# Optimization experiments

Hardware: AMD Instinct MI355X
Metric: run time of the kernel (lower is better)

The kernel has to match this reference:

```python
import math
import jax, jax.numpy as jnp
import numpy as np

SIZES = (32.0, 64.0, 128.0, 256.0, 512.0)
RATIOS = (0.5, 1.0, 2.0)
STRIDE = 16.0
IMG_SIZE = 1600.0
PRE_NMS = 2000
POST_NMS = 1000
NMS_THRESH = 0.7
MIN_SIZE = 1e-3
BBOX_CLIP = math.log(1000.0 / 16.0)  # torchvision dw/dh clamp


def make_anchors(H, W):
    # cell anchors (AnchorsGenerator.generate_anchors)
    scales = jnp.asarray(SIZES, jnp.float32)
    h_r = jnp.sqrt(jnp.asarray(RATIOS, jnp.float32))
    w_r = 1.0 / h_r
    ws = (w_r[:, None] * scales[None, :]).reshape(-1)
    hs = (h_r[:, None] * scales[None, :]).reshape(-1)
    base = jnp.round(jnp.stack([-ws, -hs, ws, hs], 1) / 2.0)  # [A,4]
    # grid shifts (grid_anchors)
    sx = jnp.arange(W, dtype=jnp.float32) * STRIDE
    sy = jnp.arange(H, dtype=jnp.float32) * STRIDE
    yy, xx = jnp.meshgrid(sy, sx, indexing='ij')
    shifts = jnp.stack([xx.ravel(), yy.ravel(), xx.ravel(), yy.ravel()], 1)  # [HW,4]
    return (shifts[:, None, :] + base[None, :, :]).reshape(-1, 4)  # [HW*A,4]


def decode_boxes(deltas, anchors):
    # BoxCoder.decode with weights (1,1,1,1)
    wa = anchors[:, 2] - anchors[:, 0]
    ha = anchors[:, 3] - anchors[:, 1]
    cxa = anchors[:, 0] + 0.5 * wa
    cya = anchors[:, 1] + 0.5 * ha
    dx, dy = deltas[..., 0], deltas[..., 1]
    dw = jnp.minimum(deltas[..., 2], BBOX_CLIP)
    dh = jnp.minimum(deltas[..., 3], BBOX_CLIP)
    cx = dx * wa + cxa
    cy = dy * ha + cya
    w = jnp.exp(dw) * wa
    h = jnp.exp(dh) * ha
    return jnp.stack([cx - 0.5 * w, cy - 0.5 * h, cx + 0.5 * w, cy + 0.5 * h], -1)


def nms_single(boxes, scores):
    # boxes [K,4], scores [K]; scores of invalid (too-small) boxes are -1
    K = boxes.shape[0]
    order = jnp.argsort(-scores)
    b = boxes[order]
    s = scores[order]
    area = (b[:, 2] - b[:, 0]) * (b[:, 3] - b[:, 1])
    lt = jnp.maximum(b[:, None, :2], b[None, :, :2])
    rb = jnp.minimum(b[:, None, 2:], b[None, :, 2:])
    wh = jnp.clip(rb - lt, 0.0)
    inter = wh[..., 0] * wh[..., 1]
    iou = inter / (area[:, None] + area[None, :] - inter + 1e-6)
    valid = s > -0.5
    idxs = jnp.arange(K)

    def body(keep, i):
        sup = keep[i] & (iou[i] > NMS_THRESH) & (idxs > i)
        return keep & ~sup, None

    keep, _ = jax.lax.scan(body, valid, idxs)
    prio = jnp.where(keep, idxs, K)
    sel = jnp.argsort(prio)[:POST_NMS]
    kept = keep[sel]
    out_b = jnp.where(kept[:, None], b[sel], 0.0)
    out_s = jnp.where(kept, s[sel], 0.0)
    return out_b, out_s


def setup_inputs() -> dict:
    key = jax.random.key(0)
    k1, k2 = jax.random.split(key)
    objectness = jax.random.normal(k1, (8, 15, 100, 100), dtype=jnp.float32)
    bbox_deltas = jax.random.normal(k2, (8, 60, 100, 100), dtype=jnp.float32)
    return {"objectness": objectness, "bbox_deltas": bbox_deltas}


def reference(objectness, bbox_deltas):
    N, A, H, W = objectness.shape
    anchors = make_anchors(H, W)  # [HWA,4]
    # permute_and_flatten
    obj = objectness.transpose(0, 2, 3, 1).reshape(N, -1)  # [N,HWA]
    dl = bbox_deltas.reshape(N, A, 4, H, W).transpose(0, 3, 4, 1, 2).reshape(N, -1, 4)
    boxes = jnp.clip(decode_boxes(dl, anchors), 0.0, IMG_SIZE)  # clip to image
    scores = jax.nn.sigmoid(obj)
    top_s, idx = jax.lax.top_k(scores, PRE_NMS)  # pre-NMS top-k per image
    top_b = jnp.take_along_axis(boxes, idx[:, :, None], axis=1)
    # remove small boxes
    bw = top_b[..., 2] - top_b[..., 0]
    bh = top_b[..., 3] - top_b[..., 1]
    top_s = jnp.where((bw >= MIN_SIZE) & (bh >= MIN_SIZE), top_s, -1.0)
    out_b, out_s = jax.vmap(nms_single)(top_b, top_s)  # [N,POST,4],[N,POST]
    return jnp.concatenate([out_b, out_s[..., None]], -1)  # [N,POST,5]
```

## Files before the change

### kernel.cpp

```cpp
#include <hip/hip_runtime.h>
#include <math.h>

#define NIMG   8
#define NA     15
#define GH     100
#define GW     100
#define HW     10000
#define HWA    150000
#define NSLICE 12
#define F4S    3125
#define SLEN   12500
#define PRE    2000
#define POST   1000
#define CAP    4096
#define RCAP   512
#define MROWS  2048
#define B0_X   2.0f
#define NTILE  528
#define TBLK   66
#define SBINS  1024
#define SBASE  0x3F600000u
#define BBOX_CLIP_F 4.135166556742356f
#define IMGSZ  1600.0f

#define WS_PCNT   0u
#define WS_CAND   384u
#define WS_TOPB   393600u
#define WS_TOPS   649600u
#define WS_MASK   713856u

#define WAIT_VM(n) __builtin_amdgcn_s_waitcnt(((n)&15)|(((n)>>4)<<14)|0xF70)
#define WAIT_LGKM0 __builtin_amdgcn_s_waitcnt(0xC07F)

__device__ __forceinline__ void gl_lds16(const void* g, void* l) {
    __builtin_amdgcn_global_load_lds(
        (const __attribute__((address_space(1))) unsigned int*)g,
        (__attribute__((address_space(3))) unsigned int*)l, 16, 0, 0);
}

__device__ __forceinline__ float ref_exp_f32(float x) {
    return (float)exp((double)x);
}
__device__ __forceinline__ float ref_sigmoid(float x) {
    float t = ref_exp_f32(-x);
    return __fdiv_rn(1.0f, __fadd_rn(1.0f, t));
}

__device__ __forceinline__ float rlf(float v, int l) {
    return __int_as_float(__builtin_amdgcn_readlane(__float_as_int(v), l));
}
__device__ __forceinline__ unsigned long long rl64(unsigned long long v, int l) {
    unsigned lo = (unsigned)__builtin_amdgcn_readlane((int)(unsigned)v, l);
    unsigned hi = (unsigned)__builtin_amdgcn_readlane((int)(unsigned)(v >> 32), l);
    return ((unsigned long long)hi << 32) | (unsigned long long)lo;
}

__device__ __forceinline__ unsigned long long mk_key(float x, int e) {
    unsigned sb = __float_as_uint(ref_sigmoid(x));
    unsigned j = (unsigned)((e % HW) * NA + e / HW);
    return ((unsigned long long)sb << 32) | (unsigned long long)(0xFFFFFFFFu - j);
}

__device__ __forceinline__ void bitonic2048(unsigned long long* a, int tid) {
    for (int k = 2; k <= 2048; k <<= 1) {
        for (int j = k >> 1; j > 0; j >>= 1) {
            if (j >= 128) __syncthreads();
            int p = tid;
            int t = ((p & ~(j - 1)) << 1) | (p & (j - 1));
            int ixj = t | j;
            unsigned long long x = a[t], y = a[ixj];
            bool up = (t & k) == 0;
            if (up ? (x < y) : (x > y)) { a[t] = y; a[ixj] = x; }
            if (j >= 128) __syncthreads();
        }
    }
}

__global__ void __launch_bounds__(1024) k_scan(
        const float* __restrict__ obj,
        unsigned long long* __restrict__ cand,
        unsigned* __restrict__ pcnt) {
    __shared__ unsigned long long lbuf[RCAP];
    __shared__ unsigned lcnt_sh;
    const int n = blockIdx.x, slice = blockIdx.y, tid = threadIdx.x;
    if (tid == 0) lcnt_sh = 0u;
    __syncthreads();
    const float4* op4 = (const float4*)(obj + (size_t)n * HWA) + (size_t)slice * F4S;
    const int ebase = slice * SLEN;
    float4 v0 = op4[tid];
    float4 v1 = op4[tid + 1024];
    float4 v2 = op4[tid + 2048];
    bool tl = (tid + 3072) < F4S;
    float4 v3 = tl ? op4[tid + 3072] : make_float4(-9.f, -9.f, -9.f, -9.f);
    float xs[16] = {v0.x, v0.y, v0.z, v0.w, v1.x, v1.y, v1.z, v1.w,
                    v2.x, v2.y, v2.z, v2.w, v3.x, v3.y, v3.z, v3.w};
    #pragma unroll
    for (int q = 0; q < 16; ++q) {
        float x = xs[q];
        if (x > B0_X) {
            int e = ebase + (tid + (q >> 2) * 1024) * 4 + (q & 3);
            unsigned p = atomicAdd(&lcnt_sh, 1u);
            if (p < RCAP) lbuf[p] = mk_key(x, e);
        }
    }
    __syncthreads();
    const int r = n * NSLICE + slice;
    const unsigned L = lcnt_sh;
    if (tid == 0) pcnt[r] = L;
    const unsigned Lc = (L < RCAP) ? L : RCAP;
    unsigned long long* cp = cand + (size_t)r * RCAP;
    for (unsigned t = tid; t < Lc; t += 1024) cp[t] = lbuf[t];
}

__global__ void __launch_bounds__(1024) k_sort_decode(
        const float* __restrict__ obj,
        const unsigned* __restrict__ pcnt,
        const unsigned long long* __restrict__ cand,
        const float* __restrict__ deltas,
        float* __restrict__ topb,
        float* __restrict__ tops) {
    __shared__ unsigned long long sk[CAP];
    __shared__ unsigned long long sk2[2048];
    __shared__ unsigned shist[SBINS];
    __shared__ unsigned sstart[SBINS];
    __shared__ unsigned lcnt_sh, thr_sh, sel_sh;
    __shared__ int fb_sh, off_sh[NSLICE + 1];
    const int n = blockIdx.x, tid = threadIdx.x;
    if (tid == 0) lcnt_sh = 0u;
    if (tid < NSLICE) off_sh[tid + 1] = (int)pcnt[n * NSLICE + tid];
    for (int t = tid; t < SBINS; t += 1024) shist[t] = 0u;
    __syncthreads();
    if (tid == 0) {
        int fb = 0, acc = 0;
        off_sh[0] = 0;
        for (int s = 0; s < NSLICE; ++s) {
            int c = off_sh[s + 1];
            if (c > RCAP) fb = 1;
            acc += (c > RCAP) ? RCAP : c;
            off_sh[s + 1] = acc;
        }
        if (acc > CAP || acc < PRE) fb = 1;
        fb_sh = fb;
    }
    __syncthreads();
    int C;
    if (!fb_sh) {
        C = off_sh[NSLICE];
        for (int s = 0; s < NSLICE; ++s) {
            const int o = off_sh[s], cs = off_sh[s + 1] - o;
            const unsigned long long* cp = cand + (size_t)(n * NSLICE + s) * RCAP;
            for (int t = tid; t < cs; t += 1024) sk[o + t] = cp[t];
        }
    } else {
        const float* op = obj + (size_t)n * HWA;
        for (int e = tid; e < HWA; e += 1024) {
            float x = op[e];
            if (x > B0_X) {
                unsigned p = atomicAdd(&lcnt_sh, 1u);
                if (p < CAP) sk[p] = mk_key(x, e);
            }
        }
        __syncthreads();
        C = (int)((lcnt_sh < CAP) ? lcnt_sh : CAP);
    }
    __syncthreads();

    const unsigned long long* kp;
    if (C <= 2048) {
        for (int t = C + tid; t < 2048; t += 1024) sk[t] = 0ull;
        __syncthreads();
        bitonic2048(sk, tid);
        kp = sk;
    } else {
        for (int t = tid; t < C; t += 1024) {
            unsigned sb = (unsigned)(sk[t] >> 32);
            unsigned b = (sb - SBASE) >> 11;
            if (b > SBINS - 1) b = SBINS - 1;
            atomicAdd(&shist[b], 1u);
        }
        __syncthreads();
        if (tid < 64) {
            const int lane = tid;
            unsigned v[16]; unsigned S = 0;
            #pragma unroll
            for (int t = 0; t < 16; ++t) { v[t] = shist[lane * 16 + t]; S += v[t]; }
            unsigned T = S;
            #pragma unroll
            for (int d = 1; d < 64; d <<= 1) {
                unsigned u = __shfl_down(T, d);
                if (lane + d < 64) T += u;
            }
            unsigned running = T - S;
            int bestt = -1; unsigned bestW = 0;
            #pragma unroll
            for (int t = 15; t >= 0; --t) {
                sstart[lane * 16 + t] = running;
                running += v[t];
                if (bestt < 0 && running >= PRE) { bestt = t; bestW = running; }
            }
            unsigned long long hm = __ballot(bestt >= 0);
            int hl = 63 - __builtin_clzll(hm);
            int bt = __builtin_amdgcn_readlane(bestt, hl);
            unsigned sw = (unsigned)__builtin_amdgcn_readlane((int)bestW, hl);
            if (lane == 0) {
                thr_sh = SBASE + ((unsigned)(hl * 16 + bt) << 11);
                sel_sh = sw;
            }
        }
        __syncthreads();
        const unsigned sel = sel_sh;
        if (sel <= 2048u) {
            const unsigned thr = thr_sh;
            for (int t = tid; t < SBINS; t += 1024) shist[t] = 0u;
            __syncthreads();
            for (int t = tid; t < C; t += 1024) {
                unsigned long long key = sk[t];
                unsigned sb = (unsigned)(key >> 32);
                if (sb >= thr) {
                    unsigned b = (sb - SBASE) >> 11;
                    if (b > SBINS - 1) b = SBINS - 1;
                    unsigned p = sstart[b] + atomicAdd(&shist[b], 1u);
                    sk2[p] = key;
                }
            }
            for (unsigned t = sel + tid; t < 2048u; t += 1024) sk2[t] = 0ull;
            __syncthreads();
            for (int b = tid; b < SBINS; b += 1024) {
                int c = (int)shist[b];
                if (c > 1) {
                    int o = (int)sstart[b];
                    for (int i = 1; i < c; ++i) {
                        unsigned long long key = sk2[o + i];
                        int m = o + i - 1;
                        while (m >= o && sk2[m] < key) { sk2[m + 1] = sk2[m]; --m; }
                        sk2[m + 1] = key;
                    }
                }
            }
            __syncthreads();
            kp = sk2;
        } else {
            for (int t = C + tid; t < CAP; t += 1024) sk[t] = 0ull;
            __syncthreads();
            for (int k = 2; k <= CAP; k <<= 1) {
                for (int j = k >> 1; j > 0; j >>= 1) {
                    if (j >= 128) __syncthreads();
                    #pragma unroll
                    for (int it = 0; it < 2; ++it) {
                        int p = tid + it * 1024;
                        int t = ((p & ~(j - 1)) << 1) | (p & (j - 1));
                        int ixj = t | j;
                        unsigned long long a = sk[t], b = sk[ixj];
                        bool up = (t & k) == 0;
                        if (up ? (a < b) : (a > b)) { sk[t] = b; sk[ixj] = a; }
                    }
                    if (j >= 128) __syncthreads();
                }
            }
            kp = sk;
        }
    }
    __syncthreads();
    const float* dp = deltas + (size_t)n * (NA * 4 * HW);
    for (int t = tid; t < PRE; t += 1024) {
        unsigned long long key = kp[t];
        float* tb = topb + ((size_t)n * PRE + t) * 4;
        if (key == 0ull) {
            tb[0] = 0.f; tb[1] = 0.f; tb[2] = 0.f; tb[3] = 0.f;
            tops[(size_t)n * PRE + t] = -1.0f;
            continue;
        }
        unsigned sb = (unsigned)(key >> 32);
        unsigned j  = 0xFFFFFFFFu - (unsigned)(key & 0xFFFFFFFFull);
        float s = __uint_as_float(sb);
        int a  = (int)(j % NA), hw = (int)(j / NA);
        int gy = hw / GW, gx = hw % GW;
        int r  = a / 5, si = a % 5;
        float ratio = (r == 0) ? 0.5f : ((r == 1) ? 1.0f : 2.0f);
        float hr = __fsqrt_rn(ratio);
        float wr = __fdiv_rn(1.0f, hr);
        float scale = (float)(32 << si);
        float wsz = __fmul_rn(wr, scale);
        float hsz = __fmul_rn(hr, scale);
        float bx1 = rintf(__fmul_rn(-wsz, 0.5f));
        float by1 = rintf(__fmul_rn(-hsz, 0.5f));
        float bx2 = rintf(__fmul_rn(wsz, 0.5f));
        float by2 = rintf(__fmul_rn(hsz, 0.5f));
        float sx = (float)(gx * 16), sy = (float)(gy * 16);
        float ax1 = sx + bx1, ay1 = sy + by1, ax2 = sx + bx2, ay2 = sy + by2;
        float wa = __fsub_rn(ax2, ax1), ha = __fsub_rn(ay2, ay1);
        float cxa = __fadd_rn(ax1, __fmul_rn(0.5f, wa));
        float cya = __fadd_rn(ay1, __fmul_rn(0.5f, ha));
        int off = gy * GW + gx;
        float dx = dp[(a * 4 + 0) * HW + off];
        float dy = dp[(a * 4 + 1) * HW + off];
        float dw = fminf(dp[(a * 4 + 2) * HW + off], BBOX_CLIP_F);
        float dh = fminf(dp[(a * 4 + 3) * HW + off], BBOX_CLIP_F);
        float cx = __fadd_rn(__fmul_rn(dx, wa), cxa);
        float cy = __fadd_rn(__fmul_rn(dy, ha), cya);
        float bw = __fmul_rn(ref_exp_f32(dw), wa);
        float bh = __fmul_rn(ref_exp_f32(dh), ha);
        float hbw = __fmul_rn(0.5f, bw), hbh = __fmul_rn(0.5f, bh);
        float x1 = fminf(fmaxf(__fsub_rn(cx, hbw), 0.0f), IMGSZ);
        float y1 = fminf(fmaxf(__fsub_rn(cy, hbh), 0.0f), IMGSZ);
        float x2 = fminf(fmaxf(__fadd_rn(cx, hbw), 0.0f), IMGSZ);
        float y2 = fminf(fmaxf(__fadd_rn(cy, hbh), 0.0f), IMGSZ);
        tb[0] = x1; tb[1] = y1; tb[2] = x2; tb[3] = y2;
        bool valid = (__fsub_rn(x2, x1) >= 1e-3f) && (__fsub_rn(y2, y1) >= 1e-3f);
        tops[(size_t)n * PRE + t] = valid ? s : -1.0f;
    }
}

__global__ void __launch_bounds__(256) k_iou(
        const float* __restrict__ topb,
        unsigned long long* __restrict__ mask) {
    const int n = blockIdx.x;
    const int wid = blockIdx.y * 4 + (threadIdx.x >> 6);
    const int lane = threadIdx.x & 63;
    const float4* tb4 = (const float4*)(topb + (size_t)n * PRE * 4);
    for (int t = wid; t < NTILE; t += TBLK * 4) {
        int ti = 0, rem = t;
        while (rem >= 32 - ti) { rem -= 32 - ti; ++ti; }
        const int tj = ti + rem;
        const int i0 = ti * 64, j0 = tj * 64;
        float4 bi = tb4[i0 + lane];
        float4 bj = tb4[j0 + lane];
        float aj = __fmul_rn(__fsub_rn(bj.z, bj.x), __fsub_rn(bj.w, bj.y));
        float ai = __fmul_rn(__fsub_rn(bi.z, bi.x), __fsub_rn(bi.w, bi.y));
        const bool jlim = (j0 + lane) < PRE;
        const bool diag = (ti == tj);
        unsigned long long mval = 0ull;
        #pragma unroll 4
        for (int r = 0; r < 64; ++r) {
            float sx1 = rlf(bi.x, r), sy1 = rlf(bi.y, r);
            float sx2 = rlf(bi.z, r), sy2 = rlf(bi.w, r);
            float sa  = rlf(ai, r);
            float ltx = fmaxf(sx1, bj.x), lty = fmaxf(sy1, bj.y);
            float rbx = fminf(sx2, bj.z), rby = fminf(sy2, bj.w);
            float ww = fmaxf(__fsub_rn(rbx, ltx), 0.0f);
            float hh = fmaxf(__fsub_rn(rby, lty), 0.0f);
            float inter = __fmul_rn(ww, hh);
            float denom = __fadd_rn(__fsub_rn(__fadd_rn(sa, aj), inter), 1e-6f);
            bool bit = jlim && (!diag || lane > r) &&
                       (__fdiv_rn(inter, denom) > 0.7f);
            unsigned long long m = __ballot(bit);
            if (lane == r) mval = m;
        }
        mask[((size_t)n * MROWS + i0 + lane) * 32 + tj] = mval;
    }
}

__global__ void __launch_bounds__(256) k_nms_out(
        const float* __restrict__ topb,
        const float* __restrict__ tops,
        const unsigned long long* __restrict__ mask,
        float* __restrict__ out) {
    __shared__ unsigned long long sbuf[4][2048];
    __shared__ float sval[2048];
    __shared__ unsigned short kept[POST];
    __shared__ int cnt;
    const int n = blockIdx.x, tid = threadIdx.x;
    const float* sp = tops + (size_t)n * PRE;
    if (tid < 64) {
        const int lane = tid;
        const unsigned long long* mb = mask + (size_t)n * MROWS * 32;
        #pragma unroll
        for (int k = 0; k < 8; ++k)
            gl_lds16((const char*)sp + k * 1024 + lane * 16, (char*)sval + k * 1024);
        #pragma unroll
        for (int gg = 0; gg < 3; ++gg) {
            const char* gb = (const char*)(mb + (size_t)gg * 64 * 32);
            #pragma unroll
            for (int k = 0; k < 16; ++k)
                gl_lds16(gb + k * 1024 + lane * 16,
                         (char*)&sbuf[gg][0] + k * 1024);
        }
        WAIT_VM(48);
        unsigned long long vbit = 0ull;
        #pragma unroll
        for (int w = 0; w < 32; ++w) {
            int i = w * 64 + lane;
            bool v = (i < PRE) && (sval[i] > -0.5f);
            unsigned long long m = __ballot(v);
            if (lane == w) vbit = m;
        }
        {
            const char* gb = (const char*)(mb + (size_t)3 * 64 * 32);
            #pragma unroll
            for (int k = 0; k < 16; ++k)
                gl_lds16(gb + k * 1024 + lane * 16, (char*)&sbuf[3][0] + k * 1024);
        }
        WAIT_VM(32);
        unsigned long long rrp = sbuf[0][(size_t)lane * 32 + 0];

        unsigned long long remv = 0ull;
        int kc = 0;
        for (int g = 0; g < 32; ++g) {
            const int base = g * 64;
            WAIT_VM(32);
            const unsigned long long* sb = sbuf[g & 3];
            unsigned long long rr = rrp;
            if (g + 1 < 32)
                rrp = sbuf[(g + 1) & 3][(size_t)lane * 32 + (g + 1)];
            unsigned long long nz = __ballot(rr != 0ull);
            unsigned long long cc = rl64(remv, g);
            unsigned long long vb = rl64(vbit, g);
            unsigned long long todo = vb & ~cc;
            unsigned long long kb = 0ull;
            unsigned long long hot = todo & nz;
            while (hot) {
                int f = (int)__builtin_ctzll(hot);
                unsigned long long fbit = 1ull << f;
                unsigned long long upto = fbit | (fbit - 1ull);
                kb |= todo & upto;
                unsigned long long sup = rl64(rr, f);
                todo &= ~upto & ~sup;
                hot = todo & nz;
            }
            kb |= todo;
            if (kb) {
                if ((kb >> lane) & 1ull) {
                    int rank = __popcll(kb & ((1ull << lane) - 1ull));
                    int pos = kc + rank;
                    if (pos < POST) kept[pos] = (unsigned short)(base + lane);
                }
                kc += __popcll(kb);
            }
            if (kc >= POST || g == 31) break;
            if (kb) {
                int h = lane >> 5, c = lane & 31;
                unsigned kbl = (unsigned)(h ? (kb >> 32) : kb);
                unsigned long long acc = 0ull;
                #pragma unroll
                for (int q = 0; q < 32; ++q) {
                    unsigned long long v = sb[(h * 32 + q) * 32 + c];
                    acc |= ((kbl >> q) & 1u) ? v : 0ull;
                }
                acc |= __shfl(acc, lane ^ 32);
                remv |= acc;
            }
            WAIT_LGKM0;
            if (g + 4 < 32) {
                const char* gb = (const char*)(mb + (size_t)(g + 4) * 64 * 32);
                char* lb = (char*)&sbuf[g & 3][0];
                #pragma unroll
                for (int k = 0; k < 16; ++k)
                    gl_lds16(gb + k * 1024 + lane * 16, lb + k * 1024);
            }
        }
        if (lane == 0) cnt = (kc < POST) ? kc : POST;
    }
    __syncthreads();
    const int kc = cnt;
    for (int rI = tid; rI < POST; rI += 256) {
        float o0 = 0.f, o1 = 0.f, o2 = 0.f, o3 = 0.f, o4 = 0.f;
        if (rI < kc) {
            int i = kept[rI];
            const float* tb = topb + ((size_t)n * PRE + i) * 4;
            o0 = tb[0]; o1 = tb[1]; o2 = tb[2]; o3 = tb[3]; o4 = sval[i];
        }
        float* op = out + ((size_t)n * POST + rI) * 5;
        op[0] = o0; op[1] = o1; op[2] = o2; op[3] = o3; op[4] = o4;
    }
}

extern "C" void kernel_launch(void* const* d_in, const int* in_sizes, int n_in,
                              void* d_out, int out_size, void* d_ws, size_t ws_size,
                              hipStream_t stream) {
    const float* obj    = (const float*)d_in[0];
    const float* deltas = (const float*)d_in[1];
    float* out = (float*)d_out;
    char* ws = (char*)d_ws;

    unsigned*            pcnt  = (unsigned*)(ws + WS_PCNT);
    unsigned long long*  cand  = (unsigned long long*)(ws + WS_CAND);
    float*               topb  = (float*)(ws + WS_TOPB);
    float*               tops  = (float*)(ws + WS_TOPS);
    unsigned long long*  mask  = (unsigned long long*)(ws + WS_MASK);

    k_scan       <<<dim3(NIMG, NSLICE), 1024, 0, stream>>>(obj, cand, pcnt);
    k_sort_decode<<<NIMG, 1024, 0, stream>>>(obj, pcnt, cand, deltas, topb, tops);
    k_iou        <<<dim3(NIMG, TBLK), 256, 0, stream>>>(topb, mask);
    k_nms_out    <<<NIMG, 256, 0, stream>>>(topb, tops, mask, out);
}
```

Before: 157.6 us.

## Fuse scan, sort/decode and IoU into one redundant per-image front kernel

Merges the sliced objectness scan, the top-k sort/decode and the IoU mask kernel into a single kernel launched with 32 blocks per image. Each block redundantly rescans the whole image, sorts and decodes the top 2000 boxes into shared memory, then computes its share of the IoU tiles from LDS. Only block 0 writes topb/tops. Sigmoid is now applied only to the candidates that pass the threshold, not inside the atomic scan loop. This removes two kernel launches and the global round-trips for candidates and boxes, but it repeats the full scan and sort 32 times per image. It also drops the sliced parallel scan, so each block reads all 150000 objectness values by itself.

```diff
diff --git a/kernel.cpp b/kernel.cpp
--- a/kernel.cpp
+++ b/kernel.cpp
@@ -7,24 +7,19 @@
 #define GW     100
 #define HW     10000
 #define HWA    150000
-#define NSLICE 12
-#define F4S    3125
-#define SLEN   12500
+#define F4TOT  37500
 #define PRE    2000
 #define POST   1000
 #define CAP    4096
-#define RCAP   512
 #define MROWS  2048
 #define B0_X   2.0f
 #define NTILE  528
-#define TBLK   66
+#define BSLOTS 32
 #define SBINS  1024
 #define SBASE  0x3F600000u
 #define BBOX_CLIP_F 4.135166556742356f
 #define IMGSZ  1600.0f
 
-#define WS_PCNT   0u
-#define WS_CAND   384u
 #define WS_TOPB   393600u
 #define WS_TOPS   649600u
 #define WS_MASK   713856u
@@ -53,12 +48,6 @@
     unsigned lo = (unsigned)__builtin_amdgcn_readlane((int)(unsigned)v, l);
     unsigned hi = (unsigned)__builtin_amdgcn_readlane((int)(unsigned)(v >> 32), l);
     return ((unsigned long long)hi << 32) | (unsigned long long)lo;
-}
-
-__device__ __forceinline__ unsigned long long mk_key(float x, int e) {
-    unsigned sb = __float_as_uint(ref_sigmoid(x));
-    unsigned j = (unsigned)((e % HW) * NA + e / HW);
-    return ((unsigned long long)sb << 32) | (unsigned long long)(0xFFFFFFFFu - j);
 }
 
 __device__ __forceinline__ void bitonic2048(unsigned long long* a, int tid) {
@@ -76,92 +65,49 @@
     }
 }
 
-__global__ void __launch_bounds__(1024) k_scan(
+__global__ void __launch_bounds__(1024) k_front(
         const float* __restrict__ obj,
-        unsigned long long* __restrict__ cand,
-        unsigned* __restrict__ pcnt) {
-    __shared__ unsigned long long lbuf[RCAP];
-    __shared__ unsigned lcnt_sh;
-    const int n = blockIdx.x, slice = blockIdx.y, tid = threadIdx.x;
-    if (tid == 0) lcnt_sh = 0u;
-    __syncthreads();
-    const float4* op4 = (const float4*)(obj + (size_t)n * HWA) + (size_t)slice * F4S;
-    const int ebase = slice * SLEN;
-    float4 v0 = op4[tid];
-    float4 v1 = op4[tid + 1024];
-    float4 v2 = op4[tid + 2048];
-    bool tl = (tid + 3072) < F4S;
-    float4 v3 = tl ? op4[tid + 3072] : make_float4(-9.f, -9.f, -9.f, -9.f);
-    float xs[16] = {v0.x, v0.y, v0.z, v0.w, v1.x, v1.y, v1.z, v1.w,
-                    v2.x, v2.y, v2.z, v2.w, v3.x, v3.y, v3.z, v3.w};
-    #pragma unroll
-    for (int q = 0; q < 16; ++q) {
-        float x = xs[q];
-        if (x > B0_X) {
-            int e = ebase + (tid + (q >> 2) * 1024) * 4 + (q & 3);
-            unsigned p = atomicAdd(&lcnt_sh, 1u);
-            if (p < RCAP) lbuf[p] = mk_key(x, e);
-        }
-    }
-    __syncthreads();
-    const int r = n * NSLICE + slice;
-    const unsigned L = lcnt_sh;
-    if (tid == 0) pcnt[r] = L;
-    const unsigned Lc = (L < RCAP) ? L : RCAP;
-    unsigned long long* cp = cand + (size_t)r * RCAP;
-    for (unsigned t = tid; t < Lc; t += 1024) cp[t] = lbuf[t];
-}
-
-__global__ void __launch_bounds__(1024) k_sort_decode(
-        const float* __restrict__ obj,
-        const unsigned* __restrict__ pcnt,
-        const unsigned long long* __restrict__ cand,
         const float* __restrict__ deltas,
         float* __restrict__ topb,
-        float* __restrict__ tops) {
+        float* __restrict__ tops,
+        unsigned long long* __restrict__ mask) {
     __shared__ unsigned long long sk[CAP];
     __shared__ unsigned long long sk2[2048];
     __shared__ unsigned shist[SBINS];
     __shared__ unsigned sstart[SBINS];
+    __shared__ float4 boxes[2048];
     __shared__ unsigned lcnt_sh, thr_sh, sel_sh;
-    __shared__ int fb_sh, off_sh[NSLICE + 1];
-    const int n = blockIdx.x, tid = threadIdx.x;
+    const int n = blockIdx.x, bslot = blockIdx.y, tid = threadIdx.x;
+
     if (tid == 0) lcnt_sh = 0u;
-    if (tid < NSLICE) off_sh[tid + 1] = (int)pcnt[n * NSLICE + tid];
     for (int t = tid; t < SBINS; t += 1024) shist[t] = 0u;
     __syncthreads();
-    if (tid == 0) {
-        int fb = 0, acc = 0;
-        off_sh[0] = 0;
-        for (int s = 0; s < NSLICE; ++s) {
-            int c = off_sh[s + 1];
-            if (c > RCAP) fb = 1;
-            acc += (c > RCAP) ? RCAP : c;
-            off_sh[s + 1] = acc;
-        }
-        if (acc > CAP || acc < PRE) fb = 1;
-        fb_sh = fb;
-    }
-    __syncthreads();
-    int C;
-    if (!fb_sh) {
-        C = off_sh[NSLICE];
-        for (int s = 0; s < NSLICE; ++s) {
-            const int o = off_sh[s], cs = off_sh[s + 1] - o;
-            const unsigned long long* cp = cand + (size_t)(n * NSLICE + s) * RCAP;
-            for (int t = tid; t < cs; t += 1024) sk[o + t] = cp[t];
-        }
-    } else {
-        const float* op = obj + (size_t)n * HWA;
-        for (int e = tid; e < HWA; e += 1024) {
-            float x = op[e];
-            if (x > B0_X) {
-                unsigned p = atomicAdd(&lcnt_sh, 1u);
-                if (p < CAP) sk[p] = mk_key(x, e);
-            }
-        }
-        __syncthreads();
-        C = (int)((lcnt_sh < CAP) ? lcnt_sh : CAP);
+    {
+        const float4* op4 = (const float4*)(obj + (size_t)n * HWA);
+        for (int i4 = tid; i4 < F4TOT; i4 += 1024) {
+            float4 v = op4[i4];
+            float xs[4] = {v.x, v.y, v.z, v.w};
+            #pragma unroll
+            for (int q = 0; q < 4; ++q) {
+                float x = xs[q];
+                if (x > B0_X) {
+                    int e = i4 * 4 + q;
+                    unsigned j = (unsigned)((e % HW) * NA + e / HW);
+                    unsigned p = atomicAdd(&lcnt_sh, 1u);
+                    if (p < CAP)
+                        sk[p] = ((unsigned long long)__float_as_uint(x) << 32)
+                              | (unsigned long long)(0xFFFFFFFFu - j);
+                }
+            }
+        }
+    }
+    __syncthreads();
+    const int C = (int)((lcnt_sh < CAP) ? lcnt_sh : CAP);
+    for (int t = tid; t < C; t += 1024) {
+        unsigned long long k = sk[t];
+        float x = __uint_as_float((unsigned)(k >> 32));
+        unsigned sb = __float_as_uint(ref_sigmoid(x));
+        sk[t] = ((unsigned long long)sb << 32) | (k & 0xFFFFFFFFull);
     }
     __syncthreads();
 
@@ -174,9 +120,9 @@
     } else {
         for (int t = tid; t < C; t += 1024) {
             unsigned sb = (unsigned)(sk[t] >> 32);
-            unsigned b = (sb - SBASE) >> 11;
-            if (b > SBINS - 1) b = SBINS - 1;
-            atomicAdd(&shist[b], 1u);
+            unsigned bb = (sb - SBASE) >> 11;
+            if (bb > SBINS - 1) bb = SBINS - 1;
+            atomicAdd(&shist[bb], 1u);
         }
         __syncthreads();
         if (tid < 64) {
@@ -217,18 +163,18 @@
                 unsigned long long key = sk[t];
                 unsigned sb = (unsigned)(key >> 32);
                 if (sb >= thr) {
-                    unsigned b = (sb - SBASE) >> 11;
-                    if (b > SBINS - 1) b = SBINS - 1;
-                    unsigned p = sstart[b] + atomicAdd(&shist[b], 1u);
+                    unsigned bb = (sb - SBASE) >> 11;
+                    if (bb > SBINS - 1) bb = SBINS - 1;
+                    unsigned p = sstart[bb] + atomicAdd(&shist[bb], 1u);
                     sk2[p] = key;
                 }
             }
             for (unsigned t = sel + tid; t < 2048u; t += 1024) sk2[t] = 0ull;
             __syncthreads();
-            for (int b = tid; b < SBINS; b += 1024) {
-                int c = (int)shist[b];
+            for (int bb = tid; bb < SBINS; bb += 1024) {
+                int c = (int)shist[bb];
                 if (c > 1) {
-                    int o = (int)sstart[b];
+                    int o = (int)sstart[bb];
                     for (int i = 1; i < c; ++i) {
                         unsigned long long key = sk2[o + i];
                         int m = o + i - 1;
@@ -250,9 +196,9 @@
                         int p = tid + it * 1024;
                         int t = ((p & ~(j - 1)) << 1) | (p & (j - 1));
                         int ixj = t | j;
-                        unsigned long long a = sk[t], b = sk[ixj];
+                        unsigned long long a = sk[t], bb = sk[ixj];
                         bool up = (t & k) == 0;
-                        if (up ? (a < b) : (a > b)) { sk[t] = b; sk[ixj] = a; }
+                        if (up ? (a < bb) : (a > bb)) { sk[t] = bb; sk[ixj] = a; }
                     }
                     if (j >= 128) __syncthreads();
                 }
@@ -261,13 +207,18 @@
         }
     }
     __syncthreads();
+
+    const bool writer = (bslot == 0);
     const float* dp = deltas + (size_t)n * (NA * 4 * HW);
     for (int t = tid; t < PRE; t += 1024) {
         unsigned long long key = kp[t];
-        float* tb = topb + ((size_t)n * PRE + t) * 4;
         if (key == 0ull) {
-            tb[0] = 0.f; tb[1] = 0.f; tb[2] = 0.f; tb[3] = 0.f;
-            tops[(size_t)n * PRE + t] = -1.0f;
+            boxes[t] = make_float4(0.f, 0.f, 0.f, 0.f);
+            if (writer) {
+                float* tb = topb + ((size_t)n * PRE + t) * 4;
+                tb[0] = 0.f; tb[1] = 0.f; tb[2] = 0.f; tb[3] = 0.f;
+                tops[(size_t)n * PRE + t] = -1.0f;
+            }
             continue;
         }
         unsigned sb = (unsigned)(key >> 32);
@@ -305,48 +256,51 @@
         float y1 = fminf(fmaxf(__fsub_rn(cy, hbh), 0.0f), IMGSZ);
         float x2 = fminf(fmaxf(__fadd_rn(cx, hbw), 0.0f), IMGSZ);
         float y2 = fminf(fmaxf(__fadd_rn(cy, hbh), 0.0f), IMGSZ);
-        tb[0] = x1; tb[1] = y1; tb[2] = x2; tb[3] = y2;
-        bool valid = (__fsub_rn(x2, x1) >= 1e-3f) && (__fsub_rn(y2, y1) >= 1e-3f);
-        tops[(size_t)n * PRE + t] = valid ? s : -1.0f;
-    }
-}
-
-__global__ void __launch_bounds__(256) k_iou(
-        const float* __restrict__ topb,
-        unsigned long long* __restrict__ mask) {
-    const int n = blockIdx.x;
-    const int wid = blockIdx.y * 4 + (threadIdx.x >> 6);
-    const int lane = threadIdx.x & 63;
-    const float4* tb4 = (const float4*)(topb + (size_t)n * PRE * 4);
-    for (int t = wid; t < NTILE; t += TBLK * 4) {
-        int ti = 0, rem = t;
-        while (rem >= 32 - ti) { rem -= 32 - ti; ++ti; }
-        const int tj = ti + rem;
-        const int i0 = ti * 64, j0 = tj * 64;
-        float4 bi = tb4[i0 + lane];
-        float4 bj = tb4[j0 + lane];
-        float aj = __fmul_rn(__fsub_rn(bj.z, bj.x), __fsub_rn(bj.w, bj.y));
-        float ai = __fmul_rn(__fsub_rn(bi.z, bi.x), __fsub_rn(bi.w, bi.y));
-        const bool jlim = (j0 + lane) < PRE;
-        const bool diag = (ti == tj);
-        unsigned long long mval = 0ull;
-        #pragma unroll 4
-        for (int r = 0; r < 64; ++r) {
-            float sx1 = rlf(bi.x, r), sy1 = rlf(bi.y, r);
-            float sx2 = rlf(bi.z, r), sy2 = rlf(bi.w, r);
-            float sa  = rlf(ai, r);
-            float ltx = fmaxf(sx1, bj.x), lty = fmaxf(sy1, bj.y);
-            float rbx = fminf(sx2, bj.z), rby = fminf(sy2, bj.w);
-            float ww = fmaxf(__fsub_rn(rbx, ltx), 0.0f);
-            float hh = fmaxf(__fsub_rn(rby, lty), 0.0f);
-            float inter = __fmul_rn(ww, hh);
-            float denom = __fadd_rn(__fsub_rn(__fadd_rn(sa, aj), inter), 1e-6f);
-            bool bit = jlim && (!diag || lane > r) &&
-                       (__fdiv_rn(inter, denom) > 0.7f);
-            unsigned long long m = __ballot(bit);
-            if (lane == r) mval = m;
-        }
-        mask[((size_t)n * MROWS + i0 + lane) * 32 + tj] = mval;
+        boxes[t] = make_float4(x1, y1, x2, y2);
+        if (writer) {
+            float* tb = topb + ((size_t)n * PRE + t) * 4;
+            tb[0] = x1; tb[1] = y1; tb[2] = x2; tb[3] = y2;
+            bool valid = (__fsub_rn(x2, x1) >= 1e-3f) && (__fsub_rn(y2, y1) >= 1e-3f);
+            tops[(size_t)n * PRE + t] = valid ? s : -1.0f;
+        }
+    }
+    for (int t = PRE + tid; t < 2048; t += 1024)
+        boxes[t] = make_float4(0.f, 0.f, 0.f, 0.f);
+    __syncthreads();
+
+    {
+        const int wid = bslot * 16 + (tid >> 6);
+        const int lane = tid & 63;
+        for (int t = wid; t < NTILE; t += BSLOTS * 16) {
+            int ti = 0, rem = t;
+            while (rem >= 32 - ti) { rem -= 32 - ti; ++ti; }
+            const int tj = ti + rem;
+            const int i0 = ti * 64, j0 = tj * 64;
+            float4 bi = boxes[i0 + lane];
+            float4 bj = boxes[j0 + lane];
+            float aj = __fmul_rn(__fsub_rn(bj.z, bj.x), __fsub_rn(bj.w, bj.y));
+            float ai = __fmul_rn(__fsub_rn(bi.z, bi.x), __fsub_rn(bi.w, bi.y));
+            const bool jlim = (j0 + lane) < PRE;
+            const bool diag = (ti == tj);
+            unsigned long long mval = 0ull;
+            #pragma unroll 4
+            for (int r = 0; r < 64; ++r) {
+                float sx1 = rlf(bi.x, r), sy1 = rlf(bi.y, r);
+                float sx2 = rlf(bi.z, r), sy2 = rlf(bi.w, r);
+                float sa  = rlf(ai, r);
+                float ltx = fmaxf(sx1, bj.x), lty = fmaxf(sy1, bj.y);
+                float rbx = fminf(sx2, bj.z), rby = fminf(sy2, bj.w);
+                float ww = fmaxf(__fsub_rn(rbx, ltx), 0.0f);
+                float hh = fmaxf(__fsub_rn(rby, lty), 0.0f);
+                float inter = __fmul_rn(ww, hh);
+                float denom = __fadd_rn(__fsub_rn(__fadd_rn(sa, aj), inter), 1e-6f);
+                bool bit = jlim && (!diag || lane > r) &&
+                           (__fdiv_rn(inter, denom) > 0.7f);
+                unsigned long long m = __ballot(bit);
+                if (lane == r) mval = m;
+            }
+            mask[((size_t)n * MROWS + i0 + lane) * 32 + tj] = mval;
+        }
     }
 }
 
@@ -472,14 +426,10 @@
     float* out = (float*)d_out;
     char* ws = (char*)d_ws;
 
-    unsigned*            pcnt  = (unsigned*)(ws + WS_PCNT);
-    unsigned long long*  cand  = (unsigned long long*)(ws + WS_CAND);
     float*               topb  = (float*)(ws + WS_TOPB);
     float*               tops  = (float*)(ws + WS_TOPS);
     unsigned long long*  mask  = (unsigned long long*)(ws + WS_MASK);
 
-    k_scan       <<<dim3(NIMG, NSLICE), 1024, 0, stream>>>(obj, cand, pcnt);
-    k_sort_decode<<<NIMG, 1024, 0, stream>>>(obj, pcnt, cand, deltas, topb, tops);
-    k_iou        <<<dim3(NIMG, TBLK), 256, 0, stream>>>(topb, mask);
-    k_nms_out    <<<NIMG, 256, 0, stream>>>(topb, tops, mask, out);
-}
+    k_front  <<<dim3(NIMG, BSLOTS), 1024, 0, stream>>>(obj, deltas, topb, tops, mask);
+    k_nms_out<<<NIMG, 256, 0, stream>>>(topb, tops, mask, out);
+}
```

Result: slower. 176.2 us (+11.8%).

## Replace per-bin insertion sort with rank sort, flatten gather, drop IoU division

Applied to the files above, without the earlier changes.

Candidate gathering now runs as one flat loop over all slices, with each thread computing its slice from the prefix offsets. The serial insertion sort inside each histogram bin is replaced by a parallel rank-by-count scatter into the other buffer, using a new per-element bin index array. The IoU threshold test drops the correctly rounded float division and instead compares inter against an exact double-precision multiple of denom, with the constant chosen to reproduce the fp32 rounding boundary. The rank sort does O(c^2) comparisons per bin and uses extra shared memory. The double arithmetic may be slow on hardware with limited FP64 throughput, and the tail zero-fill of sk2 is removed.

```diff
diff --git a/kernel.cpp b/kernel.cpp
--- a/kernel.cpp
+++ b/kernel.cpp
@@ -123,6 +123,7 @@
     __shared__ unsigned long long sk2[2048];
     __shared__ unsigned shist[SBINS];
     __shared__ unsigned sstart[SBINS];
+    __shared__ unsigned short binof[2048];
     __shared__ unsigned lcnt_sh, thr_sh, sel_sh;
     __shared__ int fb_sh, off_sh[NSLICE + 1];
     const int n = blockIdx.x, tid = threadIdx.x;
@@ -146,10 +147,11 @@
     int C;
     if (!fb_sh) {
         C = off_sh[NSLICE];
-        for (int s = 0; s < NSLICE; ++s) {
-            const int o = off_sh[s], cs = off_sh[s + 1] - o;
-            const unsigned long long* cp = cand + (size_t)(n * NSLICE + s) * RCAP;
-            for (int t = tid; t < cs; t += 1024) sk[o + t] = cp[t];
+        for (int g = tid; g < C; g += 1024) {
+            int s = 0;
+            #pragma unroll
+            for (int q = 1; q < NSLICE; ++q) s += (g >= off_sh[q]);
+            sk[g] = cand[(size_t)(n * NSLICE + s) * RCAP + (g - off_sh[s])];
         }
     } else {
         const float* op = obj + (size_t)n * HWA;
@@ -221,24 +223,22 @@
                     if (b > SBINS - 1) b = SBINS - 1;
                     unsigned p = sstart[b] + atomicAdd(&shist[b], 1u);
                     sk2[p] = key;
+                    binof[p] = (unsigned short)b;
                 }
             }
-            for (unsigned t = sel + tid; t < 2048u; t += 1024) sk2[t] = 0ull;
             __syncthreads();
-            for (int b = tid; b < SBINS; b += 1024) {
+            for (unsigned t = tid; t < sel; t += 1024) {
+                unsigned long long key = sk2[t];
+                int b = (int)binof[t];
+                int o = (int)sstart[b];
                 int c = (int)shist[b];
-                if (c > 1) {
-                    int o = (int)sstart[b];
-                    for (int i = 1; i < c; ++i) {
-                        unsigned long long key = sk2[o + i];
-                        int m = o + i - 1;
-                        while (m >= o && sk2[m] < key) { sk2[m + 1] = sk2[m]; --m; }
-                        sk2[m + 1] = key;
-                    }
-                }
+                int rank = 0;
+                for (int i = 0; i < c; ++i)
+                    rank += (sk2[o + i] > key);
+                sk[o + rank] = key;
             }
             __syncthreads();
-            kp = sk2;
+            kp = sk;
         } else {
             for (int t = C + tid; t < CAP; t += 1024) sk[t] = 0ull;
             __syncthreads();
@@ -315,6 +315,7 @@
         const float* __restrict__ topb,
         unsigned long long* __restrict__ mask) {
     const int n = blockIdx.x;
+    const double M = 23488103.0 / 33554432.0;
     const int wid = blockIdx.y * 4 + (threadIdx.x >> 6);
     const int lane = threadIdx.x & 63;
     const float4* tb4 = (const float4*)(topb + (size_t)n * PRE * 4);
@@ -342,7 +343,7 @@
             float inter = __fmul_rn(ww, hh);
             float denom = __fadd_rn(__fsub_rn(__fadd_rn(sa, aj), inter), 1e-6f);
             bool bit = jlim && (!diag || lane > r) &&
-                       (__fdiv_rn(inter, denom) > 0.7f);
+                       ((double)inter >= M * (double)denom);
             unsigned long long m = __ballot(bit);
             if (lane == r) mval = m;
         }
```

Result: faster. 145.1 us (-7.9%).
